# Optimization experiments

Measured on AMD Instinct MI355X. Metric: run time of the kernel, lower is better.

## Reference

```python
import jax, jax.numpy as jnp
import numpy as np

N_VERTS = 5000
N_FACES = 10000
BATCH = 2
N_PTS = 8192
OUTER_LOOP = 4
INNER_LOOP = 50
SOLVE_SCALE = 10.0
ADAM_LR = 0.01
B1, B2, EPS = 0.9, 0.999, 1e-8


def _normalize(x, eps=1e-12):
    # torch.nn.functional.normalize(p=2, dim=-1)
    n = jnp.linalg.norm(x, axis=-1, keepdims=True)
    return x / jnp.maximum(n, eps)


def _interp_bary(tri, vw):
    # tri: [M,3,3] per-point triangle attributes, vw: [M,2] barycentric (u,v)
    bary = jnp.concatenate([vw, 1.0 - vw[:, :1] - vw[:, 1:2]], axis=-1)  # [M,3]
    return jnp.einsum('mij,mi->mj', tri, bary)


def _solve_delta_vwd(qV, fid, vw, mesh_V, mesh_F, mesh_N):
    # Newton-like correspondence solve via unrolled Adam (solve_delta_vwd).
    tri_idx = mesh_F[fid]          # [M,3]
    tri_V = mesh_V[tri_idx]        # [M,3,3]
    tri_N = mesh_N[tri_idx]        # [M,3,3]
    d0 = jnp.linalg.norm(_interp_bary(tri_V, vw) - qV, axis=-1)
    delta0 = jnp.concatenate([jnp.zeros_like(vw), d0[:, None]], axis=-1)  # [M,3]
    target = qV * SOLVE_SCALE

    def loss_fn(delta):
        w = vw + delta[:, :2]
        cV = _interp_bary(tri_V, w) * SOLVE_SCALE
        cN = _normalize(_interp_bary(tri_N, w)) * SOLVE_SCALE
        match = cV + cN * delta[:, 2:3]
        return jnp.mean((match - target) ** 2)  # F.mse_loss

    def step(carry, t):
        delta, m, v = carry
        g = jax.grad(loss_fn)(delta)
        m = B1 * m + (1.0 - B1) * g
        v = B2 * v + (1.0 - B2) * g * g
        mhat = m / (1.0 - B1 ** t)
        vhat = v / (1.0 - B2 ** t)
        delta = delta - ADAM_LR * mhat / (jnp.sqrt(vhat) + EPS)
        return (delta, m, v), None

    ts = jnp.arange(1, INNER_LOOP + 1, dtype=qV.dtype)
    zeros = jnp.zeros_like(delta0)
    (delta, _, _), _ = jax.lax.scan(step, (delta0, zeros, zeros), ts)
    return delta


def _forward(verts, mesh_V, mesh_N, mesh_F):
    b, n, _ = verts.shape
    # init_corres_spt: KNN (K=1) of query points against triangle centers
    centers = mesh_V[mesh_F].mean(axis=1)  # [F,3]
    d2 = ((verts ** 2).sum(-1)[..., None]
          + (centers ** 2).sum(-1)[None, None, :]
          - 2.0 * jnp.einsum('bnd,fd->bnf', verts, centers))  # [b,n,F]
    fidx = jnp.argmin(d2, axis=-1)                             # [b,n]
    fid = fidx.reshape(-1)
    qV = verts.reshape(-1, 3)
    vw = jnp.full((b * n, 2), 1.0 / 3.0, dtype=verts.dtype)
    # update_corres_spt (method='uvd'): outer triwalk loop.
    # triwalk is an external CPU mesh-walker; we use the module's documented
    # fallback when triwalk is None: vw <- vw + delta (face index unchanged).
    for _ in range(OUTER_LOOP):
        delta = _solve_delta_vwd(qV, fid, vw, mesh_V, mesh_F, mesh_N)
        vw = vw + delta[:, :2]
    outlier_mask = jnp.zeros((b, n), dtype=bool)  # max_dist = inf
    return fidx, vw.reshape(b, n, 2), outlier_mask


def setup_inputs() -> dict:
    key = jax.random.key(0)
    k1, k2, k3, k4 = jax.random.split(key, 4)
    mesh_V = jax.random.normal(k1, (N_VERTS, 3), dtype=jnp.float32)
    mesh_F = jax.random.randint(k2, (N_FACES, 3), 0, N_VERTS)
    mesh_N = _normalize(jax.random.normal(k3, (N_VERTS, 3), dtype=jnp.float32))
    verts = jax.random.normal(k4, (BATCH, N_PTS, 3), dtype=jnp.float32)
    return {"verts": verts, "mesh_V": mesh_V, "mesh_N": mesh_N, "mesh_F": mesh_F}


def reference(verts, mesh_V, mesh_N, mesh_F):
    return _forward(verts, mesh_V, mesh_N, mesh_F)
```

## Files before the change

kernel.cpp:

```cpp
#include <hip/hip_runtime.h>
#include <math.h>
#include <stdint.h>

constexpr int kVerts = 5000;
constexpr int kFaces = 10000;
constexpr int kPts   = 16384;
constexpr int kOuter = 4;
constexpr int kInner = 50;

#define SCALE 10.0f

#define KNN_WAVES 16
#define KNN_FQ    4
constexpr int kQuarter     = kFaces / KNN_FQ;
constexpr int kChunk       = kQuarter / 2;
constexpr int kPtsPerLane  = 4;
constexpr int kPtsPerBlock = 64 * kPtsPerLane;
constexpr int kPtGroups    = kPts / kPtsPerBlock;

typedef float v2f __attribute__((ext_vector_type(2)));

__device__ __forceinline__ v2f pk_mul(v2f a, v2f b) {
    v2f d; asm("v_pk_mul_f32 %0, %1, %2" : "=v"(d) : "v"(a), "v"(b)); return d;
}
__device__ __forceinline__ v2f pk_add(v2f a, v2f b) {
    v2f d; asm("v_pk_add_f32 %0, %1, %2" : "=v"(d) : "v"(a), "v"(b)); return d;
}

struct BiasTabP { float rb[kInner + 2][2]; };
constexpr BiasTabP make_tabp() {
    BiasTabP t{};
    float b1 = 1.0f, b2 = 1.0f;
    for (int i = 0; i < kInner; ++i) {
        b1 *= 0.9f; b2 *= 0.999f;
        t.rb[i][0] = 1.0f / (1.0f - b1);
        t.rb[i][1] = 1.0f / (1.0f - b2);
    }
    t.rb[kInner][0]     = t.rb[kInner - 1][0];
    t.rb[kInner][1]     = t.rb[kInner - 1][1];
    t.rb[kInner + 1][0] = t.rb[kInner - 1][0];
    t.rb[kInner + 1][1] = t.rb[kInner - 1][1];
    return t;
}
constexpr BiasTabP kTabP = make_tabp();

__global__ __launch_bounds__(256)
void centers_kernel(const float* __restrict__ mesh_V,
                    const int*   __restrict__ mesh_F,
                    float*       __restrict__ soa)
{
    const int f = blockIdx.x * 256 + threadIdx.x;
    if (f >= kFaces) return;
    const int i0 = mesh_F[f * 3 + 0];
    const int i1 = mesh_F[f * 3 + 1];
    const int i2 = mesh_F[f * 3 + 2];
    const float cx = __fdiv_rn(__fadd_rn(__fadd_rn(mesh_V[i0*3+0], mesh_V[i1*3+0]), mesh_V[i2*3+0]), 3.0f);
    const float cy = __fdiv_rn(__fadd_rn(__fadd_rn(mesh_V[i0*3+1], mesh_V[i1*3+1]), mesh_V[i2*3+1]), 3.0f);
    const float cz = __fdiv_rn(__fadd_rn(__fadd_rn(mesh_V[i0*3+2], mesh_V[i1*3+2]), mesh_V[i2*3+2]), 3.0f);
    const float cc = __fadd_rn(__fadd_rn(__fmul_rn(cx, cx), __fmul_rn(cy, cy)),
                               __fmul_rn(cz, cz));
    soa[0 * kFaces + f] = cx;
    soa[1 * kFaces + f] = cy;
    soa[2 * kFaces + f] = cz;
    soa[3 * kFaces + f] = cc;
}

__global__ __launch_bounds__(1024)
void knn_kernel(const float* __restrict__ verts,
                const float* __restrict__ soa,
                float*       __restrict__ ws_d2,
                int*         __restrict__ ws_f)
{
    __shared__ float s_soa[4][kChunk];
    __shared__ float s_best [KNN_WAVES][kPtsPerBlock];
    __shared__ int   s_bestf[KNN_WAVES][kPtsPerBlock];

    const int tid  = threadIdx.x;
    const int lane = tid & 63;
    const int wv   = __builtin_amdgcn_readfirstlane(tid >> 6);
    const int pg   = blockIdx.x >> 2;
    const int fq   = blockIdx.x & 3;
    const int qbeg = fq * kQuarter;

    v2f ndx[kPtsPerLane], ndy[kPtsPerLane], ndz[kPtsPerLane], q2p[kPtsPerLane];
#pragma unroll
    for (int k = 0; k < kPtsPerLane; ++k) {
        const int p = pg * kPtsPerBlock + k * 64 + lane;
        const float qx = verts[p * 3 + 0];
        const float qy = verts[p * 3 + 1];
        const float qz = verts[p * 3 + 2];
        const float q2 = __fadd_rn(__fadd_rn(__fmul_rn(qx, qx), __fmul_rn(qy, qy)),
                                   __fmul_rn(qz, qz));
        const float nx = -__fmul_rn(2.0f, qx);
        const float ny = -__fmul_rn(2.0f, qy);
        const float nz = -__fmul_rn(2.0f, qz);
        ndx[k] = (v2f){nx, nx};
        ndy[k] = (v2f){ny, ny};
        ndz[k] = (v2f){nz, nz};
        q2p[k] = (v2f){q2, q2};
    }

    float bd0[kPtsPerLane], bd1[kPtsPerLane];
    int   bf0[kPtsPerLane], bf1[kPtsPerLane];
#pragma unroll
    for (int k = 0; k < kPtsPerLane; ++k) {
        bd0[k] = INFINITY;   bd1[k] = INFINITY;
        bf0[k] = 0x7fffffff; bf1[k] = 0x7fffffff;
    }

    const int fbeg = 2 * ((wv * (kChunk / 2)) / KNN_WAVES);
    const int fend = 2 * (((wv + 1) * (kChunk / 2)) / KNN_WAVES);

    for (int c = 0; c < 2; ++c) {
        const int cbase = qbeg + c * kChunk;

        for (int o = tid; o < 4 * (kChunk / 2); o += 1024) {
            const int comp = o / (kChunk / 2);
            const int idx  = o - comp * (kChunk / 2);
            const v2f val = *reinterpret_cast<const v2f*>(soa + comp * kFaces + cbase + 2 * idx);
            *reinterpret_cast<v2f*>(&s_soa[comp][2 * idx]) = val;
        }
        __syncthreads();

#pragma unroll 2
        for (int f = fbeg; f < fend; f += 2) {
            const v2f cx2 = *reinterpret_cast<const v2f*>(&s_soa[0][f]);
            const v2f cy2 = *reinterpret_cast<const v2f*>(&s_soa[1][f]);
            const v2f cz2 = *reinterpret_cast<const v2f*>(&s_soa[2][f]);
            const v2f cw2 = *reinterpret_cast<const v2f*>(&s_soa[3][f]);
            const int gf  = cbase + f;
#pragma unroll
            for (int k = 0; k < kPtsPerLane; ++k) {
                const v2f m0   = pk_mul(ndx[k], cx2);
                const v2f m1   = pk_mul(ndy[k], cy2);
                const v2f m2   = pk_mul(ndz[k], cz2);
                const v2f s01  = pk_add(m0, m1);
                const v2f dotn = pk_add(s01, m2);
                const v2f qc   = pk_add(q2p[k], cw2);
                const v2f d2   = pk_add(qc, dotn);
                if (d2.x < bd0[k]) { bd0[k] = d2.x; bf0[k] = gf; }
                if (d2.y < bd1[k]) { bd1[k] = d2.y; bf1[k] = gf + 1; }
            }
        }
        __syncthreads();
    }

#pragma unroll
    for (int k = 0; k < kPtsPerLane; ++k) {
        if (bd1[k] < bd0[k] || (bd1[k] == bd0[k] && bf1[k] < bf0[k])) {
            bd0[k] = bd1[k]; bf0[k] = bf1[k];
        }
        s_best [wv][k * 64 + lane] = bd0[k];
        s_bestf[wv][k * 64 + lane] = bf0[k];
    }
    __syncthreads();

    if (tid < kPtsPerBlock) {
        float best  = s_best [0][tid];
        int   bestf = s_bestf[0][tid];
#pragma unroll
        for (int w = 1; w < KNN_WAVES; ++w) {
            const float ob = s_best [w][tid];
            const int   of = s_bestf[w][tid];
            if (ob < best || (ob == best && of < bestf)) { best = ob; bestf = of; }
        }
        const int p = pg * kPtsPerBlock + tid;
        ws_d2[fq * kPts + p] = best;
        ws_f [fq * kPts + p] = bestf;
    }
}

template<int K>
__device__ __forceinline__ float qbcast(float v) {
    return __int_as_float(__builtin_amdgcn_update_dpp(
        0, __float_as_int(v), K * 0x55 , 0xF, 0xF, true));
}

__global__ __launch_bounds__(256)
void solve_kernel(const float* __restrict__ verts,
                  const float* __restrict__ mesh_V,
                  const float* __restrict__ mesh_N,
                  const int*   __restrict__ mesh_F,
                  const float* __restrict__ ws_d2,
                  const int*   __restrict__ ws_f,
                  float*       __restrict__ out)
{
    const int t  = blockIdx.x * 256 + threadIdx.x;
    const int p  = t >> 2;
    const int ch = t & 3;
    const bool isV = (ch == 1);
    const bool isD = (ch >= 2);

    float bdm = ws_d2[p];
    int   f   = ws_f[p];
#pragma unroll
    for (int q = 1; q < KNN_FQ; ++q) {
        const float d  = ws_d2[q * kPts + p];
        const int   ff = ws_f [q * kPts + p];
        if (d < bdm) { bdm = d; f = ff; }
    }
    if (ch == 0) out[p] = (float)f;

    const float qx = verts[p * 3 + 0];
    const float qy = verts[p * 3 + 1];
    const float qz = verts[p * 3 + 2];

    const int i0 = mesh_F[f * 3 + 0];
    const int i1 = mesh_F[f * 3 + 1];
    const int i2 = mesh_F[f * 3 + 2];

    const float V0x = mesh_V[i0*3+0], V0y = mesh_V[i0*3+1], V0z = mesh_V[i0*3+2];
    const float V1x = mesh_V[i1*3+0], V1y = mesh_V[i1*3+1], V1z = mesh_V[i1*3+2];
    const float V2x = mesh_V[i2*3+0], V2y = mesh_V[i2*3+1], V2z = mesh_V[i2*3+2];
    const float N0x = mesh_N[i0*3+0], N0y = mesh_N[i0*3+1], N0z = mesh_N[i0*3+2];
    const float N1x = mesh_N[i1*3+0], N1y = mesh_N[i1*3+1], N1z = mesh_N[i1*3+2];
    const float N2x = mesh_N[i2*3+0], N2y = mesh_N[i2*3+1], N2z = mesh_N[i2*3+2];

    const float E0x = V0x - V2x, E0y = V0y - V2y, E0z = V0z - V2z;
    const float E1x = V1x - V2x, E1y = V1y - V2y, E1z = V1z - V2z;
    const float F0x = N0x - N2x, F0y = N0y - N2y, F0z = N0z - N2z;
    const float F1x = N1x - N2x, F1y = N1y - N2y, F1z = N1z - N2z;

    const float Aux = isV ? E1x : E0x;
    const float Auy = isV ? E1y : E0y;
    const float Auz = isV ? E1z : E0z;
    const float Bx  = isD ? 0.0f : (isV ? F1x : F0x);
    const float By  = isD ? 0.0f : (isV ? F1y : F0y);
    const float Bz  = isD ? 0.0f : (isV ? F1z : F0z);

    const float tx = qx * SCALE, ty = qy * SCALE, tz = qz * SCALE;
    const float GS = 2.0f / (3.0f * 16384.0f);
    const float B1c = 0.9f,  ONE_M_B1 = 1.0f - 0.9f;
    const float B2c = 0.999f, ONE_M_B2 = 1.0f - 0.999f;

    float vwu = 1.0f / 3.0f, vwv = 1.0f / 3.0f;

#define SOLVE_STEP(RB1, RB2)                                                   \
    {                                                                          \
        const float du = qbcast<0>(dlt);                                       \
        const float dv = qbcast<1>(dlt);                                       \
        const float dd = qbcast<2>(dlt);                                       \
        const float bu = vwu + du;                                             \
        const float bv = vwv + dv;                                             \
        const float bw = (1.0f - bu) - bv;                                     \
        const float cVx = ((bu * V0x + bv * V1x) + bw * V2x) * SCALE;          \
        const float cVy = ((bu * V0y + bv * V1y) + bw * V2y) * SCALE;          \
        const float cVz = ((bu * V0z + bv * V1z) + bw * V2z) * SCALE;          \
        const float nrx = (bu * N0x + bv * N1x) + bw * N2x;                    \
        const float nry = (bu * N0y + bv * N1y) + bw * N2y;                    \
        const float nrz = (bu * N0z + bv * N1z) + bw * N2z;                    \
        const float nn  = (nrx * nrx + nry * nry) + nrz * nrz;                 \
        const float inv = __builtin_amdgcn_rsqf(nn);                           \
        const float nhx = nrx * inv, nhy = nry * inv, nhz = nrz * inv;         \
        const float cNx = nhx * SCALE, cNy = nhy * SCALE, cNz = nhz * SCALE;   \
        const float rx = (cVx + cNx * dd) - tx;                                \
        const float ry = (cVy + cNy * dd) - ty;                                \
        const float rz = (cVz + cNz * dd) - tz;                                \
        const float Ax = isD ? nhx : Aux;                                      \
        const float Ay = isD ? nhy : Auy;                                      \
        const float Az = isD ? nhz : Auz;                                      \
        const float dotA = (rx * Ax + ry * Ay) + rz * Az;                      \
        const float dotB = (rx * Bx + ry * By) + rz * Bz;                      \
        const float nhB  = (nhx * Bx + nhy * By) + nhz * Bz;                   \
        const float nr_r = qbcast<2>(dotA);                                    \
        const float g = GS * (SCALE * dotA + (dd * SCALE) * ((dotB - nr_r * nhB) * inv)); \
        mA = B1c * mA + ONE_M_B1 * g;                                          \
        vA = B2c * vA + ONE_M_B2 * (g * g);                                    \
        const float s = __builtin_amdgcn_rsqf(vA * (RB2) + 1e-16f);            \
        dlt -= 0.01f * (mA * (RB1)) * s;                                       \
    }

    for (int outer = 0; outer < kOuter; ++outer) {
        const float bw0 = (1.0f - vwu) - vwv;
        const float px = ((vwu * V0x + vwv * V1x) + bw0 * V2x);
        const float py = ((vwu * V0y + vwv * V1y) + bw0 * V2y);
        const float pz = ((vwu * V0z + vwv * V1z) + bw0 * V2z);
        const float dx = px - qx, dy = py - qy, dz = pz - qz;
        const float d0 = __builtin_amdgcn_sqrtf((dx * dx + dy * dy) + dz * dz);

        float dlt = isD ? d0 : 0.0f;
        float mA  = 0.0f, vA = 0.0f;

        float rbA1 = kTabP.rb[0][0], rbA2 = kTabP.rb[0][1];
        float rbB1 = kTabP.rb[1][0], rbB2 = kTabP.rb[1][1];
#pragma unroll 1
        for (int it2 = 0; it2 < kInner / 2; ++it2) {
            const float n1a = kTabP.rb[2 * it2 + 2][0];
            const float n2a = kTabP.rb[2 * it2 + 2][1];
            const float n1b = kTabP.rb[2 * it2 + 3][0];
            const float n2b = kTabP.rb[2 * it2 + 3][1];
            SOLVE_STEP(rbA1, rbA2);
            SOLVE_STEP(rbB1, rbB2);
            rbA1 = n1a; rbA2 = n2a; rbB1 = n1b; rbB2 = n2b;
        }
        vwu += qbcast<0>(dlt);
        vwv += qbcast<1>(dlt);
    }
#undef SOLVE_STEP

    if (ch == 0) {
        out[kPts + 2 * p + 0] = vwu;
        out[kPts + 2 * p + 1] = vwv;
        out[3 * kPts + p]     = 0.0f;
    }
}

extern "C" void kernel_launch(void* const* d_in, const int* in_sizes, int n_in,
                              void* d_out, int out_size, void* d_ws, size_t ws_size,
                              hipStream_t stream) {
    const float* verts  = (const float*)d_in[0];
    const float* mesh_V = (const float*)d_in[1];
    const float* mesh_N = (const float*)d_in[2];
    const int*   mesh_F = (const int*)d_in[3];
    float* out = (float*)d_out;

    float* ws_soa = (float*)d_ws;
    float* ws_d2  = (float*)((char*)d_ws + 4 * kFaces * sizeof(float));
    int*   ws_f   = (int*)((char*)ws_d2 + KNN_FQ * kPts * sizeof(float));

    hipLaunchKernelGGL(centers_kernel, dim3((kFaces + 255) / 256), dim3(256), 0, stream,
                       mesh_V, mesh_F, ws_soa);
    hipLaunchKernelGGL(knn_kernel,     dim3(kPtGroups * KNN_FQ), dim3(1024), 0, stream,
                       verts, ws_soa, ws_d2, ws_f);
    hipLaunchKernelGGL(solve_kernel,   dim3(kPts * 4 / 256), dim3(256), 0, stream,
                       verts, mesh_V, mesh_N, mesh_F, ws_d2, ws_f, out);
}
```

Measured before the change: 130.1 us.

## Load whole face quarter into interleaved float4 LDS and halve points per lane

The KNN kernel now stages its entire quarter of face centers into LDS once, in two interleaved float4 arrays, instead of in two chunks separated by barriers. The inner loop reads one pair of faces with two 128-bit LDS loads rather than four 64-bit ones. Each lane now handles 2 query points instead of 4, which doubles the number of blocks, and launch bounds request more occupancy. Less register reuse of each face load per point is traded for fewer barriers, wider LDS reads and more parallel blocks. Empty asm statements pin the splatted query vectors in registers.

```diff
diff --git a/kernel.cpp b/kernel.cpp
--- a/kernel.cpp
+++ b/kernel.cpp
@@ -13,8 +13,8 @@
 #define KNN_WAVES 16
 #define KNN_FQ    4
 constexpr int kQuarter     = kFaces / KNN_FQ;
-constexpr int kChunk       = kQuarter / 2;
-constexpr int kPtsPerLane  = 4;
+constexpr int kPairs       = kQuarter / 2;
+constexpr int kPtsPerLane  = 2;
 constexpr int kPtsPerBlock = 64 * kPtsPerLane;
 constexpr int kPtGroups    = kPts / kPtsPerBlock;
 
@@ -65,15 +65,16 @@
     soa[3 * kFaces + f] = cc;
 }
 
-__global__ __launch_bounds__(1024)
+__global__ __launch_bounds__(1024, 8)
 void knn_kernel(const float* __restrict__ verts,
                 const float* __restrict__ soa,
                 float*       __restrict__ ws_d2,
                 int*         __restrict__ ws_f)
 {
-    __shared__ float s_soa[4][kChunk];
-    __shared__ float s_best [KNN_WAVES][kPtsPerBlock];
-    __shared__ int   s_bestf[KNN_WAVES][kPtsPerBlock];
+    __shared__ float4 s_A[kPairs];
+    __shared__ float4 s_B[kPairs];
+    __shared__ float  s_best [KNN_WAVES][kPtsPerBlock];
+    __shared__ int    s_bestf[KNN_WAVES][kPtsPerBlock];
 
     const int tid  = threadIdx.x;
     const int lane = tid & 63;
@@ -81,6 +82,15 @@
     const int pg   = blockIdx.x >> 2;
     const int fq   = blockIdx.x & 3;
     const int qbeg = fq * kQuarter;
+
+    for (int p = tid; p < kPairs; p += 1024) {
+        const v2f cx2 = *reinterpret_cast<const v2f*>(soa + 0 * kFaces + qbeg + 2 * p);
+        const v2f cy2 = *reinterpret_cast<const v2f*>(soa + 1 * kFaces + qbeg + 2 * p);
+        const v2f cz2 = *reinterpret_cast<const v2f*>(soa + 2 * kFaces + qbeg + 2 * p);
+        const v2f cc2 = *reinterpret_cast<const v2f*>(soa + 3 * kFaces + qbeg + 2 * p);
+        s_A[p] = make_float4(cx2.x, cx2.y, cy2.x, cy2.y);
+        s_B[p] = make_float4(cz2.x, cz2.y, cc2.x, cc2.y);
+    }
 
     v2f ndx[kPtsPerLane], ndy[kPtsPerLane], ndz[kPtsPerLane], q2p[kPtsPerLane];
 #pragma unroll
@@ -94,10 +104,10 @@
         const float nx = -__fmul_rn(2.0f, qx);
         const float ny = -__fmul_rn(2.0f, qy);
         const float nz = -__fmul_rn(2.0f, qz);
-        ndx[k] = (v2f){nx, nx};
-        ndy[k] = (v2f){ny, ny};
-        ndz[k] = (v2f){nz, nz};
-        q2p[k] = (v2f){q2, q2};
+        ndx[k] = (v2f){nx, nx};  asm("" : "+v"(ndx[k]));
+        ndy[k] = (v2f){ny, ny};  asm("" : "+v"(ndy[k]));
+        ndz[k] = (v2f){nz, nz};  asm("" : "+v"(ndz[k]));
+        q2p[k] = (v2f){q2, q2};  asm("" : "+v"(q2p[k]));
     }
 
     float bd0[kPtsPerLane], bd1[kPtsPerLane];
@@ -108,41 +118,32 @@
         bf0[k] = 0x7fffffff; bf1[k] = 0x7fffffff;
     }
 
-    const int fbeg = 2 * ((wv * (kChunk / 2)) / KNN_WAVES);
-    const int fend = 2 * (((wv + 1) * (kChunk / 2)) / KNN_WAVES);
-
-    for (int c = 0; c < 2; ++c) {
-        const int cbase = qbeg + c * kChunk;
-
-        for (int o = tid; o < 4 * (kChunk / 2); o += 1024) {
-            const int comp = o / (kChunk / 2);
-            const int idx  = o - comp * (kChunk / 2);
-            const v2f val = *reinterpret_cast<const v2f*>(soa + comp * kFaces + cbase + 2 * idx);
-            *reinterpret_cast<v2f*>(&s_soa[comp][2 * idx]) = val;
+    __syncthreads();
+
+    const int pbeg = (wv * kPairs) / KNN_WAVES;
+    const int pend = ((wv + 1) * kPairs) / KNN_WAVES;
+
+#pragma unroll 2
+    for (int f = pbeg; f < pend; ++f) {
+        const float4 ab = s_A[f];
+        const float4 zb = s_B[f];
+        const v2f cx2 = (v2f){ab.x, ab.y};
+        const v2f cy2 = (v2f){ab.z, ab.w};
+        const v2f cz2 = (v2f){zb.x, zb.y};
+        const v2f cc2 = (v2f){zb.z, zb.w};
+        const int gf  = qbeg + 2 * f;
+#pragma unroll
+        for (int k = 0; k < kPtsPerLane; ++k) {
+            const v2f m0   = pk_mul(ndx[k], cx2);
+            const v2f m1   = pk_mul(ndy[k], cy2);
+            const v2f m2   = pk_mul(ndz[k], cz2);
+            const v2f s01  = pk_add(m0, m1);
+            const v2f dotn = pk_add(s01, m2);
+            const v2f qc   = pk_add(q2p[k], cc2);
+            const v2f d2   = pk_add(qc, dotn);
+            if (d2.x < bd0[k]) { bd0[k] = d2.x; bf0[k] = gf; }
+            if (d2.y < bd1[k]) { bd1[k] = d2.y; bf1[k] = gf + 1; }
         }
-        __syncthreads();
-
-#pragma unroll 2
-        for (int f = fbeg; f < fend; f += 2) {
-            const v2f cx2 = *reinterpret_cast<const v2f*>(&s_soa[0][f]);
-            const v2f cy2 = *reinterpret_cast<const v2f*>(&s_soa[1][f]);
-            const v2f cz2 = *reinterpret_cast<const v2f*>(&s_soa[2][f]);
-            const v2f cw2 = *reinterpret_cast<const v2f*>(&s_soa[3][f]);
-            const int gf  = cbase + f;
-#pragma unroll
-            for (int k = 0; k < kPtsPerLane; ++k) {
-                const v2f m0   = pk_mul(ndx[k], cx2);
-                const v2f m1   = pk_mul(ndy[k], cy2);
-                const v2f m2   = pk_mul(ndz[k], cz2);
-                const v2f s01  = pk_add(m0, m1);
-                const v2f dotn = pk_add(s01, m2);
-                const v2f qc   = pk_add(q2p[k], cw2);
-                const v2f d2   = pk_add(qc, dotn);
-                if (d2.x < bd0[k]) { bd0[k] = d2.x; bf0[k] = gf; }
-                if (d2.y < bd1[k]) { bd1[k] = d2.y; bf1[k] = gf + 1; }
-            }
-        }
-        __syncthreads();
     }
 
 #pragma unroll
```

Measured after the change: 128.0 us. No clear change (-1.6%).
